# Kernel tuning notes

Measured on AMD Instinct MI355X. Metric: run time of the kernel, lower is better.

## Reference

```python
import jax, jax.numpy as jnp
import numpy as np
import math

B, N, L, D = 8, 128, 30, 256


def setup_inputs() -> dict:
    key = jax.random.key(0)
    ks = jax.random.split(key, 8)
    return {
        "f_b": jax.random.normal(ks[0], (B, N, D), jnp.float32),
        "f_w": jax.random.normal(ks[1], (B, L, D), jnp.float32),
        "f_s": jax.random.normal(ks[2], (B, D), jnp.float32),
        "f_m": jax.random.normal(ks[3], (B, N, N, D), jnp.float32),
        "query_mask": jnp.ones((B, L), jnp.float32),
        "length_mask": jnp.ones((B, N), jnp.float32),
        "Wq": jax.random.normal(ks[4], (D, D), jnp.float32) / math.sqrt(D),
        "bq": jax.random.normal(ks[5], (D,), jnp.float32) * 0.02,
        "Wk": jax.random.normal(ks[6], (D, D), jnp.float32) / math.sqrt(D),
        "bk": jax.random.normal(ks[7], (D,), jnp.float32) * 0.02,
    }


def reference(f_b, f_w, f_s, f_m, query_mask, length_mask, Wq, bq, Wk, bk):
    d = f_b.shape[-1]
    scale = 1.0 / math.sqrt(d)
    NEG = -1e9

    # --- Attention(f_b over f_w) ---
    q = f_b @ Wq.T + bq                                   # [B,N,D]
    k = f_w @ Wk.T + bk                                   # [B,L,D]
    aw = jnp.einsum('bnd,bld->bnl', q, k) * scale         # [B,N,L]
    qm = query_mask[:, None, :]                           # [B,1,L]
    aw = jnp.where(qm == 0, NEG, aw * qm)
    aw = jax.nn.softmax(aw, axis=-1)
    f_baq = jnp.einsum('bnl,bld->bnd', aw, f_w)           # [B,N,D]

    fb_mask = length_mask[:, :, None]                     # [B,N,1]
    f_baq = f_baq * fb_mask
    f_bq = f_b * (f_baq + f_s[:, None, :])                # [B,N,D]

    # --- self-attention over boundary features ---
    A = jnp.einsum('bnd,bmd->bnm', f_bq, f_bq) * scale    # [B,N,N]
    lm = length_mask[:, None, :]                          # [B,1,N]
    A = jnp.where(lm == 0, NEG, A * lm)
    A = jax.nn.softmax(A, axis=-1) * fb_mask              # [B,N,N]
    f_bb = jnp.einsum('bnm,bmd->bnd', A, f_b) * fb_mask

    # --- gated aggregation over the 2D moment map ---
    g_m = jax.nn.sigmoid(f_m * f_s[:, None, None, :])     # [B,N,N,D]
    f_bm = jnp.einsum('bnm,bnmd->bnd', A, g_m * f_m)      # [B,N,D]

    return f_bb + f_b + f_bm
```

## Files before the change

### kernel.cpp

```cpp
#include <hip/hip_runtime.h>
#include <math.h>

#define B_ 8
#define N_ 128
#define L_ 30
#define D_ 256
#define NEGV -1000000000.0f
#define SCALE 0.0625f

__global__ __launch_bounds__(256) void kk2(const float* __restrict__ f_w,
    const float* __restrict__ Wk, const float* __restrict__ bk,
    const float* __restrict__ Wq, const float* __restrict__ bq,
    float* __restrict__ k2f, float* __restrict__ sv) {
  int l = blockIdx.x;
  int t = threadIdx.x, wave = t >> 6, lane = t & 63;
  __shared__ float part[4][16][65];
  __shared__ float kl[D_];
  __shared__ float wsum[4];

  float4 x4 = ((const float4*)(f_w + (size_t)l * D_))[lane];

  for (int g = 0; g < 4; ++g) {
    int dbase = wave * 64 + g * 16;
#pragma unroll
    for (int i = 0; i < 16; ++i) {
      float4 w4 = ((const float4*)(Wk + (size_t)(dbase + i) * D_))[lane];
      part[wave][i][lane] = w4.x*x4.x + w4.y*x4.y + w4.z*x4.z + w4.w*x4.w;
    }
    float s = 0.f;
#pragma unroll
    for (int j = 0; j < 16; ++j)
      s += part[wave][lane & 15][(lane >> 4) * 16 + j];
    s += __shfl_xor(s, 16);
    s += __shfl_xor(s, 32);
    if (lane < 16) kl[dbase + lane] = s + bk[dbase + lane];
  }
  __syncthreads();

  float a0 = 0.f, a1 = 0.f, a2 = 0.f, a3 = 0.f;
#pragma unroll 4
  for (int d4 = 0; d4 < 64; ++d4) {
    float4 kv = ((const float4*)kl)[d4];
    a0 += kv.x * Wq[(size_t)(4*d4+0) * D_ + t];
    a1 += kv.y * Wq[(size_t)(4*d4+1) * D_ + t];
    a2 += kv.z * Wq[(size_t)(4*d4+2) * D_ + t];
    a3 += kv.w * Wq[(size_t)(4*d4+3) * D_ + t];
  }
  k2f[(size_t)l * D_ + t] = (a0 + a1) + (a2 + a3);

  float p = bq[t] * kl[t];
#pragma unroll
  for (int off = 32; off >= 1; off >>= 1) p += __shfl_xor(p, off);
  if (lane == 0) wsum[wave] = p;
  __syncthreads();
  if (t == 0) sv[l] = wsum[0] + wsum[1] + wsum[2] + wsum[3];
}

__global__ __launch_bounds__(256) void aw_fbq(const float* __restrict__ f_b,
    const float* __restrict__ f_w, const float* __restrict__ f_s,
    const float* __restrict__ qmask, const float* __restrict__ lmask,
    const float* __restrict__ k2f, const float* __restrict__ sv,
    float* __restrict__ fbq) {
  int blk = blockIdx.x;
  int b = blk >> 5, n0 = (blk & 31) * 4;
  int t = threadIdx.x;

  __shared__ float k2l[L_][260];
  __shared__ float fbl[4][260];
  __shared__ float pdot[120][2];
  __shared__ float awl[4][32];
  __shared__ float slds[32];

  for (int r = 0; r < 4; ++r)
    fbl[r][t] = f_b[(size_t)(b * N_ + n0 + r) * D_ + t];
  for (int l = 0; l < L_; ++l)
    k2l[l][t] = k2f[(size_t)(b * L_ + l) * D_ + t];
  if (t < L_) slds[t] = sv[b * L_ + t];
  __syncthreads();

  if (t < 240) {
    int p = t % 120, half = t / 120;
    int r = p / 30, l = p % 30;
    const float4* fr = (const float4*)(fbl[r] + half * 128);
    const float4* kr = (const float4*)(k2l[l] + half * 128);
    float ac[4] = {0.f, 0.f, 0.f, 0.f};
#pragma unroll
    for (int j = 0; j < 32; ++j) {
      float4 fv = fr[j], kv = kr[j];
      ac[j & 3] += fv.x*kv.x + fv.y*kv.y + fv.z*kv.z + fv.w*kv.w;
    }
    pdot[p][half] = (ac[0] + ac[1]) + (ac[2] + ac[3]);
  }
  __syncthreads();

  if (t < 120) {
    int r = t / 30, l = t % 30;
    float acc = pdot[t][0] + pdot[t][1];
    float aw = (acc + slds[l]) * SCALE;
    float qm = qmask[b * L_ + l];
    awl[r][l] = (qm == 0.f) ? NEGV : aw * qm;
  }
  __syncthreads();

  if (t < 4) {
    float mx = -1e30f;
    for (int l = 0; l < L_; ++l) mx = fmaxf(mx, awl[t][l]);
    float s = 0.f;
    for (int l = 0; l < L_; ++l) { float e = __expf(awl[t][l] - mx); awl[t][l] = e; s += e; }
    float inv = 1.f / s;
    for (int l = 0; l < L_; ++l) awl[t][l] *= inv;
  }
  __syncthreads();

  for (int l = 0; l < L_; ++l)
    k2l[l][t] = f_w[(size_t)(b * L_ + l) * D_ + t];
  __syncthreads();

  float fsd = f_s[b * D_ + t];
  for (int r = 0; r < 4; ++r) {
    float f0 = 0.f, f1 = 0.f;
#pragma unroll
    for (int l = 0; l < L_; l += 2) {
      f0 += awl[r][l] * k2l[l][t];
      f1 += awl[r][l + 1] * k2l[l + 1][t];
    }
    float lm = lmask[b * N_ + n0 + r];
    fbq[(size_t)(b * N_ + n0 + r) * D_ + t] = fbl[r][t] * ((f0 + f1) * lm + fsd);
  }
}

__global__ __launch_bounds__(256) void fused_stream(const float* __restrict__ f_b,
    const float* __restrict__ f_m, const float* __restrict__ f_s,
    const float* __restrict__ lmask, const float* __restrict__ fbq,
    float* __restrict__ out) {
  int bn = blockIdx.x, b = bn >> 7, n = bn & 127;
  int t = threadIdx.x, w = t >> 6, lane = t & 63;

  __shared__ float part[4][32][65];
  __shared__ float a_lds[N_];
  __shared__ float sm[8];
  __shared__ float4 red[3][64];
  __shared__ float fbbred[D_];

  const float4* fmb = (const float4*)(f_m + (size_t)bn * N_ * D_);
  const float4* fbb = (const float4*)(f_b + (size_t)b * N_ * D_);
  int m0 = w * 32;

  float4 qv = ((const float4*)(fbq + (size_t)bn * D_))[lane];
#pragma unroll 8
  for (int i = 0; i < 32; ++i) {
    float4 v = ((const float4*)(fbq + (size_t)(b * N_ + m0 + i) * D_))[lane];
    part[w][i][lane] = v.x*qv.x + v.y*qv.y + v.z*qv.z + v.w*qv.w;
  }
  __builtin_amdgcn_sched_barrier(0);

  float4 pA[8], pB[8];
#pragma unroll
  for (int i = 0; i < 8; ++i) pA[i] = fmb[(size_t)(m0 + i) * 64 + lane];
#pragma unroll
  for (int i = 0; i < 8; ++i) pB[i] = fmb[(size_t)(m0 + 8 + i) * 64 + lane];
  __builtin_amdgcn_sched_barrier(0);

  __syncthreads();
  float s = 0.f;
#pragma unroll
  for (int j = 0; j < 32; ++j)
    s += part[w][lane & 31][(lane >> 5) * 32 + j];
  s += __shfl_xor(s, 32);
  if (lane < 32) a_lds[m0 + (lane & 31)] = s;
  __syncthreads();

  float lmn = lmask[b * N_ + n];
  float e = 0.f;
  if (t < N_) {
    float lm = lmask[b * N_ + t];
    float v = (lm == 0.f) ? NEGV : a_lds[t] * SCALE * lm;
    float mx = v;
#pragma unroll
    for (int off = 32; off >= 1; off >>= 1) mx = fmaxf(mx, __shfl_xor(mx, off));
    if (lane == 0) sm[w] = mx;
  }
  __syncthreads();
  if (t < N_) {
    float lm = lmask[b * N_ + t];
    float v = (lm == 0.f) ? NEGV : a_lds[t] * SCALE * lm;
    float gmax = fmaxf(sm[0], sm[1]);
    e = __expf(v - gmax);
    float ss = e;
#pragma unroll
    for (int off = 32; off >= 1; off >>= 1) ss += __shfl_xor(ss, off);
    if (lane == 0) sm[4 + w] = ss;
  }
  __syncthreads();
  if (t < N_) {
    float tot = sm[4] + sm[5];
    a_lds[t] = e * (lmn / tot);
  }
  __syncthreads();

  {
    const float* fbcol = f_b + (size_t)b * N_ * D_ + t;
    float f0 = 0.f, f1 = 0.f;
#pragma unroll 8
    for (int m = 0; m < N_; m += 2) {
      f0 += a_lds[m]     * fbcol[(size_t)m * D_];
      f1 += a_lds[m + 1] * fbcol[(size_t)(m + 1) * D_];
    }
    fbbred[t] = f0 + f1;
  }

  float4 fs4 = ((const float4*)(f_s + (size_t)b * D_))[lane];
  const float CLOG = -1.44269504088896f;
  float4 cs;
  cs.x = fs4.x * CLOG; cs.y = fs4.y * CLOG;
  cs.z = fs4.z * CLOG; cs.w = fs4.w * CLOG;
  float4 acc = make_float4(0.f, 0.f, 0.f, 0.f);

  auto compute8 = [&](float4 (&P)[8], int mbase) {
#pragma unroll
    for (int i = 0; i < 8; ++i) {
      float a = a_lds[mbase + i];
      float4 fm4 = P[i];
      float gx = __builtin_amdgcn_rcpf(1.f + __builtin_amdgcn_exp2f(fm4.x * cs.x));
      float gy = __builtin_amdgcn_rcpf(1.f + __builtin_amdgcn_exp2f(fm4.y * cs.y));
      float gz = __builtin_amdgcn_rcpf(1.f + __builtin_amdgcn_exp2f(fm4.z * cs.z));
      float gw = __builtin_amdgcn_rcpf(1.f + __builtin_amdgcn_exp2f(fm4.w * cs.w));
      acc.x += a * (gx * fm4.x);
      acc.y += a * (gy * fm4.y);
      acc.z += a * (gz * fm4.z);
      acc.w += a * (gw * fm4.w);
    }
  };

  compute8(pA, m0);
#pragma unroll
  for (int i = 0; i < 8; ++i) pA[i] = fmb[(size_t)(m0 + 16 + i) * 64 + lane];
  compute8(pB, m0 + 8);
#pragma unroll
  for (int i = 0; i < 8; ++i) pB[i] = fmb[(size_t)(m0 + 24 + i) * 64 + lane];
  compute8(pA, m0 + 16);
  compute8(pB, m0 + 24);

  if (w > 0) red[w - 1][lane] = acc;
  __syncthreads();
  if (w == 0) {
#pragma unroll
    for (int j = 0; j < 3; ++j) {
      float4 r4 = red[j][lane];
      acc.x += r4.x; acc.y += r4.y; acc.z += r4.z; acc.w += r4.w;
    }
    float4 fbn = fbb[(size_t)n * 64 + lane];
    float4 bb = ((const float4*)fbbred)[lane];
    float4 o;
    o.x = fbn.x + acc.x + lmn * bb.x;
    o.y = fbn.y + acc.y + lmn * bb.y;
    o.z = fbn.z + acc.z + lmn * bb.z;
    o.w = fbn.w + acc.w + lmn * bb.w;
    ((float4*)out)[(size_t)bn * 64 + lane] = o;
  }
}

extern "C" void kernel_launch(void* const* d_in, const int* in_sizes, int n_in,
                              void* d_out, int out_size, void* d_ws, size_t ws_size,
                              hipStream_t stream) {
  const float* f_b   = (const float*)d_in[0];
  const float* f_w   = (const float*)d_in[1];
  const float* f_s   = (const float*)d_in[2];
  const float* f_m   = (const float*)d_in[3];
  const float* qmask = (const float*)d_in[4];
  const float* lmask = (const float*)d_in[5];
  const float* Wq    = (const float*)d_in[6];
  const float* bq    = (const float*)d_in[7];
  const float* Wk    = (const float*)d_in[8];
  const float* bk    = (const float*)d_in[9];
  float* out = (float*)d_out;

  float* ws  = (float*)d_ws;
  float* k2f = ws;
  float* sv  = ws + 65536;
  float* fbq = ws + 131072;

  hipLaunchKernelGGL(kk2, dim3(B_ * L_), dim3(256), 0, stream,
                     f_w, Wk, bk, Wq, bq, k2f, sv);
  hipLaunchKernelGGL(aw_fbq, dim3(256), dim3(256), 0, stream,
                     f_b, f_w, f_s, qmask, lmask, k2f, sv, fbq);
  hipLaunchKernelGGL(fused_stream, dim3(B_ * N_), dim3(256), 0, stream,
                     f_b, f_m, f_s, lmask, fbq, out);
}
```

Measured before the change: 52.67 us.

## Stream f_m through LDS with async global_load_lds double buffering

Replaces the register-prefetched f_m loads, which were issued before the attention softmax, with per-wave double-buffered global_load_lds transfers into the reused part[] shared buffer. The loads now start only after the softmax and f_bb reduction, with a vmcnt-based wait per 4-row chunk. This is meant to lower register pressure and overlap the loads with sigmoid compute. It adds a block barrier and an LDS round trip, and it loses the early prefetch that previously overlapped with the A computation.

```diff
diff --git a/kernel.cpp b/kernel.cpp
--- a/kernel.cpp
+++ b/kernel.cpp
@@ -7,6 +7,9 @@
 #define D_ 256
 #define NEGV -1000000000.0f
 #define SCALE 0.0625f
+
+typedef const __attribute__((address_space(1))) void* as1_cvptr;
+typedef __attribute__((address_space(3))) void* as3_vptr;
 
 __global__ __launch_bounds__(256) void kk2(const float* __restrict__ f_w,
     const float* __restrict__ Wk, const float* __restrict__ bk,
@@ -136,13 +139,14 @@
   int bn = blockIdx.x, b = bn >> 7, n = bn & 127;
   int t = threadIdx.x, w = t >> 6, lane = t & 63;
 
-  __shared__ float part[4][32][65];
+  __shared__ __align__(16) float smem[4 * 32 * 65];
   __shared__ float a_lds[N_];
   __shared__ float sm[8];
   __shared__ float4 red[3][64];
   __shared__ float fbbred[D_];
 
-  const float4* fmb = (const float4*)(f_m + (size_t)bn * N_ * D_);
+  float (*part)[32][65] = (float (*)[32][65])smem;
+
   const float4* fbb = (const float4*)(f_b + (size_t)b * N_ * D_);
   int m0 = w * 32;
 
@@ -152,13 +156,6 @@
     float4 v = ((const float4*)(fbq + (size_t)(b * N_ + m0 + i) * D_))[lane];
     part[w][i][lane] = v.x*qv.x + v.y*qv.y + v.z*qv.z + v.w*qv.w;
   }
-  __builtin_amdgcn_sched_barrier(0);
-
-  float4 pA[8], pB[8];
-#pragma unroll
-  for (int i = 0; i < 8; ++i) pA[i] = fmb[(size_t)(m0 + i) * 64 + lane];
-#pragma unroll
-  for (int i = 0; i < 8; ++i) pB[i] = fmb[(size_t)(m0 + 8 + i) * 64 + lane];
   __builtin_amdgcn_sched_barrier(0);
 
   __syncthreads();
@@ -208,6 +205,7 @@
     }
     fbbred[t] = f0 + f1;
   }
+  __syncthreads();
 
   float4 fs4 = ((const float4*)(f_s + (size_t)b * D_))[lane];
   const float CLOG = -1.44269504088896f;
@@ -216,11 +214,41 @@
   cs.z = fs4.z * CLOG; cs.w = fs4.w * CLOG;
   float4 acc = make_float4(0.f, 0.f, 0.f, 0.f);
 
-  auto compute8 = [&](float4 (&P)[8], int mbase) {
-#pragma unroll
-    for (int i = 0; i < 8; ++i) {
-      float a = a_lds[mbase + i];
-      float4 fm4 = P[i];
+  float* mystage = smem + w * 2048;
+  const float* fmbase = f_m + (size_t)bn * N_ * D_;
+
+  asm volatile("s_waitcnt vmcnt(0)" ::: "memory");
+  __builtin_amdgcn_sched_barrier(0);
+
+  auto issue_chunk = [&](int c) {
+#pragma unroll
+    for (int r = 0; r < 4; ++r) {
+      const float* g = fmbase + (size_t)(m0 + c * 4 + r) * D_ + lane * 4;
+      float* lp = mystage + (c & 1) * 1024 + r * 256;
+      __builtin_amdgcn_global_load_lds((as1_cvptr)(const void*)g,
+                                       (as3_vptr)(void*)lp, 16, 0, 0);
+    }
+  };
+
+  issue_chunk(0);
+  issue_chunk(1);
+
+#pragma unroll
+  for (int c = 0; c < 8; ++c) {
+    if (c < 7) { asm volatile("s_waitcnt vmcnt(4)" ::: "memory"); }
+    else       { asm volatile("s_waitcnt vmcnt(0)" ::: "memory"); }
+    __builtin_amdgcn_sched_barrier(0);
+    const float* buf = mystage + (c & 1) * 1024;
+    float4 v[4];
+#pragma unroll
+    for (int r = 0; r < 4; ++r)
+      v[r] = *(const float4*)(buf + r * 256 + lane * 4);
+    __builtin_amdgcn_sched_barrier(0);
+    if (c + 2 < 8) issue_chunk(c + 2);
+#pragma unroll
+    for (int r = 0; r < 4; ++r) {
+      float a = a_lds[m0 + c * 4 + r];
+      float4 fm4 = v[r];
       float gx = __builtin_amdgcn_rcpf(1.f + __builtin_amdgcn_exp2f(fm4.x * cs.x));
       float gy = __builtin_amdgcn_rcpf(1.f + __builtin_amdgcn_exp2f(fm4.y * cs.y));
       float gz = __builtin_amdgcn_rcpf(1.f + __builtin_amdgcn_exp2f(fm4.z * cs.z));
@@ -230,16 +258,7 @@
       acc.z += a * (gz * fm4.z);
       acc.w += a * (gw * fm4.w);
     }
-  };
-
-  compute8(pA, m0);
-#pragma unroll
-  for (int i = 0; i < 8; ++i) pA[i] = fmb[(size_t)(m0 + 16 + i) * 64 + lane];
-  compute8(pB, m0 + 8);
-#pragma unroll
-  for (int i = 0; i < 8; ++i) pB[i] = fmb[(size_t)(m0 + 24 + i) * 64 + lane];
-  compute8(pA, m0 + 16);
-  compute8(pB, m0 + 24);
+  }
 
   if (w > 0) red[w - 1][lane] = acc;
   __syncthreads();
```

Measured after the change: 56.03 us. 6.4% more time.
